# Kernel tuning notes

Measured on AMD Instinct MI355X. Metric: run time of the kernel, lower is better.

The kernel has to match this reference:

```python
import jax, jax.numpy as jnp
import numpy as np

VOXEL_SIZE = 0.04  # metres per voxel (init_kwargs voxel_size)


def setup_inputs() -> dict:
    key = jax.random.key(0)
    k_feat, k_depth, k_zero, k_t = jax.random.split(key, 4)
    B, C, H, W = 4, 32, 120, 160
    X, Y, Z = 128, 128, 64

    features = jax.random.normal(k_feat, (B, C, H, W), dtype=jnp.float32)

    depths = jax.random.uniform(k_depth, (B, H, W), minval=0.5, maxval=5.0)
    zero_mask = jax.random.uniform(k_zero, (B, H, W)) < 0.05
    depths = jnp.where(zero_mask, 0.0, depths).astype(jnp.float32)

    # realistic post-stride intrinsics (f=200 px, principal point at centre)
    K = jnp.array([[200.0, 0.0, 80.0],
                   [0.0, 200.0, 60.0],
                   [0.0, 0.0, 1.0]], dtype=jnp.float32)
    # extrinsics: identity rotation, small per-frame translation
    t = jax.random.uniform(k_t, (B, 3), minval=-0.5, maxval=0.5)
    Rt = jnp.concatenate([jnp.tile(jnp.eye(3, dtype=jnp.float32)[None], (B, 1, 1)),
                          t[:, :, None]], axis=2)              # (B,3,4)
    projection = jnp.einsum('ij,bjk->bik', K, Rt)              # (B,3,4)

    origin = jnp.tile(jnp.array([-3.2, -3.2, 0.0], dtype=jnp.float32)[None], (B, 1))

    return {"origin": origin, "projection": projection, "features": features,
            "depths": depths, "X": X, "Y": Y, "Z": Z}


def reference(origin, projection, features, depths, X, Y, Z):
    B, C, H, W = features.shape
    HW = H * W
    XYZ = X * Y * Z

    # pixel grid: torch.meshgrid(arange(H), arange(W)) -> v over rows, u over cols
    v, u = jnp.meshgrid(jnp.arange(H, dtype=features.dtype),
                        jnp.arange(W, dtype=features.dtype), indexing='ij')
    d = depths                                                  # (B,H,W)
    uvd = jnp.stack([u[None] * d, v[None] * d, d, jnp.ones_like(d)],
                    axis=1).reshape(B, 4, HW)                   # (B,4,HW)

    # homogenise projection and invert per batch
    bottom = jnp.tile(jnp.array([[[0.0, 0.0, 0.0, 1.0]]], dtype=projection.dtype),
                      (B, 1, 1))
    proj4 = jnp.concatenate([projection, bottom], axis=1)       # (B,4,4)
    proj_inv = jnp.linalg.inv(proj4)
    world = jnp.einsum('bij,bjp->bip', proj_inv, uvd)[:, :3]    # (B,3,HW)

    voxel_id = jnp.round((world - origin[:, :, None]) / VOXEL_SIZE).astype(jnp.int32)

    depth_mask = (depths.reshape(B, HW) > 0)
    in_x = (voxel_id[:, 0] >= 0) & (voxel_id[:, 0] < X)
    in_y = (voxel_id[:, 1] >= 0) & (voxel_id[:, 1] < Y)
    in_z = (voxel_id[:, 2] >= 0) & (voxel_id[:, 2] < Z)
    mask = depth_mask & in_x & in_y & in_z                      # (B,HW)

    # flat voxel index; invalid pixels routed out-of-bounds and dropped by scatter
    lin = voxel_id[:, 0] * (Y * Z) + voxel_id[:, 1] * Z + voxel_id[:, 2]
    lin = jnp.where(mask, lin, XYZ)                             # (B,HW)

    feat_flat = features.reshape(B, C, HW)

    def scatter_one(lin_b, feat_b):
        vol = jnp.zeros((C, XYZ), dtype=features.dtype).at[:, lin_b].set(
            feat_b, mode='drop')
        val = jnp.zeros((XYZ,), dtype=features.dtype).at[lin_b].set(
            1.0, mode='drop')
        return vol, val

    volume, valid = jax.vmap(scatter_one)(lin, feat_flat)
    return volume.reshape(B, C, X, Y, Z), valid.reshape(B, 1, X, Y, Z)
```

## Files before the change

### kernel.cpp

```cpp
#include <hip/hip_runtime.h>

#define IMG_W 160
#define VOXEL 0.04f

typedef float f32x4 __attribute__((ext_vector_type(4)));

__device__ __forceinline__ void make_inv(const float* __restrict__ proj, int b,
                                         float inv[12]) {
  const float* P = proj + b * 12;
  const float p00 = P[0], p01 = P[1], p02 = P[2], p03 = P[3];
  const float p11 = P[5], p12 = P[6], p13 = P[7];
  const float p22 = P[10], p23 = P[11];
  const float i00 = __fdiv_rn(1.0f, p00);
  const float i11 = __fdiv_rn(1.0f, p11);
  const float i22 = __fdiv_rn(1.0f, p22);
  const float i01 = __fmul_rn(-i11, __fmul_rn(p01, i00));
  float x0 = __fmul_rn(p02, i00);
  x0 = __fmaf_rn(p12, i01, x0);
  const float x1 = __fmul_rn(p12, i11);
  const float i02 = __fmul_rn(-i22, x0);
  const float i12 = __fmul_rn(-i22, x1);
  float y0 = __fmul_rn(p03, i00);
  y0 = __fmaf_rn(p13, i01, y0);
  float y1 = __fmul_rn(p13, i11);
  y0 = __fmaf_rn(p23, i02, y0);
  y1 = __fmaf_rn(p23, i12, y1);
  const float y2 = __fmul_rn(p23, i22);
  inv[0] = i00;  inv[1] = i01;  inv[2] = i02;   inv[3] = -y0;
  inv[4] = 0.0f; inv[5] = i11;  inv[6] = i12;   inv[7] = -y1;
  inv[8] = 0.0f; inv[9] = 0.0f; inv[10] = i22;  inv[11] = -y2;
}

__device__ __forceinline__ int voxel_lin(const float* __restrict__ origin,
                                         const float* __restrict__ proj,
                                         float d, int b, int p,
                                         int X, int Y, int Z) {
  float inv[12];
  make_inv(proj, b, inv);
  const float u = (float)(p % IMG_W);
  const float v = (float)(p / IMG_W);
  const float uvd[4] = { __fmul_rn(u, d), __fmul_rn(v, d), d, 1.0f };
  float w[3];
#pragma unroll
  for (int r = 0; r < 3; ++r) {
    float acc = 0.0f;
#pragma unroll
    for (int j = 0; j < 4; ++j)
      acc = __fadd_rn(acc, __fmul_rn(inv[r * 4 + j], uvd[j]));
    w[r] = acc;
  }
  const float cx = __fdiv_rn(__fsub_rn(w[0], origin[b * 3 + 0]), VOXEL);
  const float cy = __fdiv_rn(__fsub_rn(w[1], origin[b * 3 + 1]), VOXEL);
  const float cz = __fdiv_rn(__fsub_rn(w[2], origin[b * 3 + 2]), VOXEL);
  const int ix = (int)rintf(cx);
  const int iy = (int)rintf(cy);
  const int iz = (int)rintf(cz);
  if (ix < 0 || ix >= X || iy < 0 || iy >= Y || iz < 0 || iz >= Z) return -1;
  return (ix * Y + iy) * Z + iz;
}

__global__ void k_winner(const float* __restrict__ origin,
                         const float* __restrict__ proj,
                         const float* __restrict__ depths,
                         const int* __restrict__ Xp, const int* __restrict__ Yp,
                         const int* __restrict__ Zp,
                         int* __restrict__ winner, int B, int HW) {
  const int gid = blockIdx.x * blockDim.x + threadIdx.x;
  if (gid >= B * HW) return;
  const int b = gid / HW;
  const int p = gid - b * HW;
  const float d = depths[gid];
  if (!(d > 0.0f)) return;
  const int X = *Xp, Y = *Yp, Z = *Zp;
  const int lin = voxel_lin(origin, proj, d, b, p, X, Y, Z);
  if (lin < 0) return;
  atomicMax(&winner[(long long)b * (X * Y * Z) + lin], p + 1);
}

__device__ __forceinline__ f32x4 vol_quad(const int4 w4,
                                          const float* __restrict__ fc) {
  f32x4 res = {0.0f, 0.0f, 0.0f, 0.0f};
  if ((w4.x | w4.y | w4.z | w4.w) != 0) {
    if (w4.x > 0) res.x = fc[w4.x - 1];
    if (w4.y > 0) res.y = fc[w4.y - 1];
    if (w4.z > 0) res.z = fc[w4.z - 1];
    if (w4.w > 0) res.w = fc[w4.w - 1];
  }
  return res;
}

__device__ __forceinline__ f32x4 val_quad(const int4 w4) {
  f32x4 vo;
  vo.x = (w4.x > 0) ? 1.0f : 0.0f;
  vo.y = (w4.y > 0) ? 1.0f : 0.0f;
  vo.z = (w4.z > 0) ? 1.0f : 0.0f;
  vo.w = (w4.w > 0) ? 1.0f : 0.0f;
  return vo;
}

__global__ void __launch_bounds__(256) k_out8(
    const float* __restrict__ feats, const int* __restrict__ winner,
    float* __restrict__ out, unsigned volFloats, unsigned totFloats,
    unsigned HW, unsigned lgXYZ, unsigned XYZm1, unsigned lgC,
    unsigned nWaves) {
  const unsigned lane = threadIdx.x & 63u;
  const unsigned wid  = (blockIdx.x * 256u + threadIdx.x) >> 6;
  if (wid >= nWaves) return;
  const unsigned q0 = wid * 512u + lane;
  int4 w[8];
#pragma unroll
  for (int k = 0; k < 8; ++k) {
    const unsigned o4 = (q0 + (unsigned)k * 64u) << 2;
    unsigned widx;
    if (o4 < volFloats) {
      const unsigned bc = o4 >> lgXYZ;
      widx = ((bc >> lgC) << lgXYZ) | (o4 & XYZm1);
    } else {
      widx = o4 - volFloats;
    }
    w[k] = *(const int4*)(winner + widx);
  }
#pragma unroll
  for (int k = 0; k < 8; ++k) {
    const unsigned o4 = (q0 + (unsigned)k * 64u) << 2;
    f32x4 res;
    if (o4 < volFloats) {
      const unsigned bc = o4 >> lgXYZ;
      res = vol_quad(w[k], feats + (size_t)bc * HW);
    } else {
      res = val_quad(w[k]);
    }
    *(f32x4*)(out + o4) = res;
  }
}

__global__ void __launch_bounds__(256) k_out(
    const float* __restrict__ feats, const int* __restrict__ winner,
    float* __restrict__ out, unsigned volQuads, unsigned totQuads,
    unsigned HW, unsigned lgXYZ, unsigned XYZm1, unsigned lgC) {
  const unsigned o = blockIdx.x * 256u + threadIdx.x;
  if (o >= totQuads) return;
  const unsigned o4 = o << 2;
  f32x4 res;
  if (o < volQuads) {
    const unsigned bc   = o4 >> lgXYZ;
    const unsigned lin0 = o4 & XYZm1;
    const unsigned b    = bc >> lgC;
    const int4 w4 = *(const int4*)(winner + (((size_t)b << lgXYZ) + lin0));
    res = vol_quad(w4, feats + (size_t)bc * HW);
  } else {
    const unsigned v0 = o4 - (volQuads << 2);
    res = val_quad(*(const int4*)(winner + v0));
  }
  *(f32x4*)(out + o4) = res;
}

extern "C" void kernel_launch(void* const* d_in, const int* in_sizes, int n_in,
                              void* d_out, int out_size, void* d_ws, size_t ws_size,
                              hipStream_t stream) {
  const float* origin = (const float*)d_in[0];
  const float* proj   = (const float*)d_in[1];
  const float* feats  = (const float*)d_in[2];
  const float* depths = (const float*)d_in[3];
  const int*   Xp     = (const int*)d_in[4];
  const int*   Yp     = (const int*)d_in[5];
  const int*   Zp     = (const int*)d_in[6];

  const int B  = in_sizes[0] / 3;
  const int HW = in_sizes[3] / B;
  const int C  = in_sizes[2] / (B * HW);
  const long long XYZ = (long long)out_size / (B * (C + 1));

  float* volume = (float*)d_out;
  int*   winner = (int*)d_ws;

  unsigned lgXYZ = 0; while ((1ll << lgXYZ) < XYZ) ++lgXYZ;
  unsigned lgC = 0;   while ((1u << lgC) < (unsigned)C) ++lgC;
  const bool pow2ok = ((XYZ & (XYZ - 1)) == 0) && ((C & (C - 1)) == 0) &&
                      (XYZ % 256 == 0) && (out_size % 4 == 0);

  hipMemsetAsync(d_ws, 0, (size_t)B * XYZ * sizeof(int), stream);

  const int total = B * HW;
  const int block = 256;
  const int grid  = (total + block - 1) / block;
  k_winner<<<grid, block, 0, stream>>>(origin, proj, depths, Xp, Yp, Zp,
                                       winner, B, HW);

  const unsigned totFloats = (unsigned)out_size;
  const unsigned volFloats = (unsigned)((long long)B * C * XYZ);
  const unsigned totQuads  = totFloats >> 2;
  if (pow2ok && (totQuads % 512u == 0)) {
    const unsigned nWaves = totQuads >> 9;
    const unsigned ogrid  = (nWaves * 64u + 255u) / 256u;
    k_out8<<<ogrid, 256, 0, stream>>>(feats, winner, volume, volFloats,
                                      totFloats, (unsigned)HW, lgXYZ,
                                      (unsigned)(XYZ - 1), lgC, nWaves);
  } else {
    const unsigned volQuads = volFloats >> 2;
    const unsigned ogrid = (totQuads + 255u) / 256u;
    k_out<<<ogrid, 256, 0, stream>>>(feats, winner, volume, volQuads,
                                     totQuads, (unsigned)HW, lgXYZ,
                                     (unsigned)(XYZ - 1), lgC);
  }
}
```

Measured before the change: 602.1 us.

## Pack winner indices to 16-bit and swizzle output blocks across XCDs

Adds a pass that narrows the 32-bit winner array to 16-bit indices, which halves the bytes the output kernel reads for each voxel. The output kernel also remaps block IDs so each XCD gets a contiguous range of blocks, aiming for better L2 locality when several channel slices re-read the same winner data. The cost is an extra kernel launch and an extra read and write of the winner array, plus a larger workspace requirement. A fallback to the 32-bit path remains when HW+1 exceeds 16 bits or the workspace is too small.

```diff
diff --git a/kernel.cpp b/kernel.cpp
--- a/kernel.cpp
+++ b/kernel.cpp
@@ -2,6 +2,7 @@
 
 #define IMG_W 160
 #define VOXEL 0.04f
+#define NXCD 8u
 
 typedef float f32x4 __attribute__((ext_vector_type(4)));
 
@@ -77,6 +78,41 @@
   atomicMax(&winner[(long long)b * (X * Y * Z) + lin], p + 1);
 }
 
+__global__ void __launch_bounds__(256) k_pack(const int* __restrict__ w32,
+                                              unsigned short* __restrict__ w16,
+                                              unsigned nquad) {
+  const unsigned i = blockIdx.x * 256u + threadIdx.x;
+  if (i >= nquad) return;
+  const int4 w = ((const int4*)w32)[i];
+  ushort4 o;
+  o.x = (unsigned short)w.x;
+  o.y = (unsigned short)w.y;
+  o.z = (unsigned short)w.z;
+  o.w = (unsigned short)w.w;
+  ((ushort4*)w16)[i] = o;
+}
+
+__device__ __forceinline__ f32x4 vol_quad_u16(const ushort4 w4,
+                                              const float* __restrict__ fc) {
+  f32x4 res = {0.0f, 0.0f, 0.0f, 0.0f};
+  if ((w4.x | w4.y | w4.z | w4.w) != 0) {
+    if (w4.x) res.x = fc[w4.x - 1];
+    if (w4.y) res.y = fc[w4.y - 1];
+    if (w4.z) res.z = fc[w4.z - 1];
+    if (w4.w) res.w = fc[w4.w - 1];
+  }
+  return res;
+}
+
+__device__ __forceinline__ f32x4 val_quad_u16(const ushort4 w4) {
+  f32x4 vo;
+  vo.x = w4.x ? 1.0f : 0.0f;
+  vo.y = w4.y ? 1.0f : 0.0f;
+  vo.z = w4.z ? 1.0f : 0.0f;
+  vo.w = w4.w ? 1.0f : 0.0f;
+  return vo;
+}
+
 __device__ __forceinline__ f32x4 vol_quad(const int4 w4,
                                           const float* __restrict__ fc) {
   f32x4 res = {0.0f, 0.0f, 0.0f, 0.0f};
@@ -96,6 +132,50 @@
   vo.z = (w4.z > 0) ? 1.0f : 0.0f;
   vo.w = (w4.w > 0) ? 1.0f : 0.0f;
   return vo;
+}
+
+__device__ __forceinline__ unsigned swz_block(unsigned o, unsigned nblk) {
+  const unsigned q = nblk / NXCD, r = nblk % NXCD;
+  const unsigned xcd = o % NXCD, idx = o / NXCD;
+  return (xcd < r) ? (xcd * (q + 1) + idx)
+                   : (r * (q + 1) + (xcd - r) * q + idx);
+}
+
+__global__ void __launch_bounds__(256) k_out8u(
+    const float* __restrict__ feats, const unsigned short* __restrict__ w16,
+    float* __restrict__ out, unsigned volFloats, unsigned totFloats,
+    unsigned HW, unsigned lgXYZ, unsigned XYZm1, unsigned lgC,
+    unsigned nWaves, unsigned nBlocks) {
+  const unsigned blk  = swz_block(blockIdx.x, nBlocks);
+  const unsigned lane = threadIdx.x & 63u;
+  const unsigned wid  = (blk * 256u + threadIdx.x) >> 6;
+  if (wid >= nWaves) return;
+  const unsigned q0 = wid * 512u + lane;
+  ushort4 w[8];
+#pragma unroll
+  for (int k = 0; k < 8; ++k) {
+    const unsigned o4 = (q0 + (unsigned)k * 64u) << 2;
+    unsigned vox;
+    if (o4 < volFloats) {
+      const unsigned bc = o4 >> lgXYZ;
+      vox = ((bc >> lgC) << lgXYZ) | (o4 & XYZm1);
+    } else {
+      vox = o4 - volFloats;
+    }
+    w[k] = ((const ushort4*)w16)[vox >> 2];
+  }
+#pragma unroll
+  for (int k = 0; k < 8; ++k) {
+    const unsigned o4 = (q0 + (unsigned)k * 64u) << 2;
+    f32x4 res;
+    if (o4 < volFloats) {
+      const unsigned bc = o4 >> lgXYZ;
+      res = vol_quad_u16(w[k], feats + (size_t)bc * HW);
+    } else {
+      res = val_quad_u16(w[k]);
+    }
+    *(f32x4*)(out + o4) = res;
+  }
 }
 
 __global__ void __launch_bounds__(256) k_out8(
@@ -173,13 +253,17 @@
 
   float* volume = (float*)d_out;
   int*   winner = (int*)d_ws;
+  const long long totvox = (long long)B * XYZ;
+  unsigned short* w16 = (unsigned short*)((char*)d_ws + (size_t)totvox * 4);
 
   unsigned lgXYZ = 0; while ((1ll << lgXYZ) < XYZ) ++lgXYZ;
   unsigned lgC = 0;   while ((1u << lgC) < (unsigned)C) ++lgC;
   const bool pow2ok = ((XYZ & (XYZ - 1)) == 0) && ((C & (C - 1)) == 0) &&
                       (XYZ % 256 == 0) && (out_size % 4 == 0);
-
-  hipMemsetAsync(d_ws, 0, (size_t)B * XYZ * sizeof(int), stream);
+  const bool u16ok  = (HW + 1 < 65536) && (totvox % 4 == 0) &&
+                      (ws_size >= (size_t)totvox * 6);
+
+  hipMemsetAsync(d_ws, 0, (size_t)totvox * sizeof(int), stream);
 
   const int total = B * HW;
   const int block = 256;
@@ -191,11 +275,20 @@
   const unsigned volFloats = (unsigned)((long long)B * C * XYZ);
   const unsigned totQuads  = totFloats >> 2;
   if (pow2ok && (totQuads % 512u == 0)) {
-    const unsigned nWaves = totQuads >> 9;
-    const unsigned ogrid  = (nWaves * 64u + 255u) / 256u;
-    k_out8<<<ogrid, 256, 0, stream>>>(feats, winner, volume, volFloats,
-                                      totFloats, (unsigned)HW, lgXYZ,
-                                      (unsigned)(XYZ - 1), lgC, nWaves);
+    const unsigned nWaves  = totQuads >> 9;
+    const unsigned nBlocks = (nWaves * 64u + 255u) / 256u;
+    if (u16ok) {
+      const unsigned nq = (unsigned)(totvox >> 2);
+      k_pack<<<(nq + 255u) / 256u, 256, 0, stream>>>(winner, w16, nq);
+      k_out8u<<<nBlocks, 256, 0, stream>>>(feats, w16, volume, volFloats,
+                                           totFloats, (unsigned)HW, lgXYZ,
+                                           (unsigned)(XYZ - 1), lgC, nWaves,
+                                           nBlocks);
+    } else {
+      k_out8<<<nBlocks, 256, 0, stream>>>(feats, winner, volume, volFloats,
+                                          totFloats, (unsigned)HW, lgXYZ,
+                                          (unsigned)(XYZ - 1), lgC, nWaves);
+    }
   } else {
     const unsigned volQuads = volFloats >> 2;
     const unsigned ogrid = (totQuads + 255u) / 256u;
```

After: 606.1 us. Within noise of the previous version (+0.7%).

## Fuse memset, winner scatter and output fill into one cooperative kernel

Applied to the files above, without the earlier changes.

Replaces the memset plus two kernel launches with a single cooperative persistent kernel of fixed grid size. It zeroes the winner buffer, runs the atomicMax scatter, and writes the output in a grid-stride loop, with grid-wide syncs between the phases. The output phase software-prefetches the next winner quad. This removes launch and inter-kernel gaps, at the cost of grid.sync overhead and fewer in-flight loads per wave than the unrolled k_out8. It falls back to the old path if the cooperative launch fails.

```diff
diff --git a/kernel.cpp b/kernel.cpp
--- a/kernel.cpp
+++ b/kernel.cpp
@@ -1,7 +1,11 @@
 #include <hip/hip_runtime.h>
+#include <hip/hip_cooperative_groups.h>
+
+namespace cg = cooperative_groups;
 
 #define IMG_W 160
 #define VOXEL 0.04f
+#define MEGA_GRID 1024
 
 typedef float f32x4 __attribute__((ext_vector_type(4)));
 
@@ -59,6 +63,109 @@
   return (ix * Y + iy) * Z + iz;
 }
 
+__device__ __forceinline__ f32x4 vol_quad(const int4 w4,
+                                          const float* __restrict__ fc) {
+  f32x4 res = {0.0f, 0.0f, 0.0f, 0.0f};
+  if ((w4.x | w4.y | w4.z | w4.w) != 0) {
+    if (w4.x > 0) res.x = fc[w4.x - 1];
+    if (w4.y > 0) res.y = fc[w4.y - 1];
+    if (w4.z > 0) res.z = fc[w4.z - 1];
+    if (w4.w > 0) res.w = fc[w4.w - 1];
+  }
+  return res;
+}
+
+__device__ __forceinline__ f32x4 val_quad(const int4 w4) {
+  f32x4 vo;
+  vo.x = (w4.x > 0) ? 1.0f : 0.0f;
+  vo.y = (w4.y > 0) ? 1.0f : 0.0f;
+  vo.z = (w4.z > 0) ? 1.0f : 0.0f;
+  vo.w = (w4.w > 0) ? 1.0f : 0.0f;
+  return vo;
+}
+
+__device__ __forceinline__ unsigned win_idx(unsigned o4, unsigned volFloats,
+                                            unsigned lgXYZ, unsigned XYZm1,
+                                            unsigned lgC) {
+  if (o4 < volFloats) {
+    const unsigned bc = o4 >> lgXYZ;
+    return ((bc >> lgC) << lgXYZ) | (o4 & XYZm1);
+  }
+  return o4 - volFloats;
+}
+
+__global__ void __launch_bounds__(256, 4) k_mega(
+    const float* __restrict__ origin, const float* __restrict__ proj,
+    const float* __restrict__ depths, const float* __restrict__ feats,
+    const int* __restrict__ Xp, const int* __restrict__ Yp,
+    const int* __restrict__ Zp, int* __restrict__ winner,
+    float* __restrict__ out, int B, int HW,
+    unsigned volFloats, unsigned totFloats, unsigned lgXYZ, unsigned XYZm1,
+    unsigned lgC, unsigned totvox) {
+  cg::grid_group grid = cg::this_grid();
+  const unsigned nthr = gridDim.x * 256u;
+  const unsigned tid  = blockIdx.x * 256u + threadIdx.x;
+
+  {
+    const unsigned nq = totvox >> 2;
+    const int4 z = make_int4(0, 0, 0, 0);
+    for (unsigned i = tid; i < nq; i += nthr) ((int4*)winner)[i] = z;
+  }
+  grid.sync();
+
+  for (unsigned g = tid; g < (unsigned)(B * HW); g += nthr) {
+    const int b = g / HW;
+    const int p = (int)g - b * HW;
+    const float d = depths[g];
+    if (d > 0.0f) {
+      const int X = *Xp, Y = *Yp, Z = *Zp;
+      const int lin = voxel_lin(origin, proj, d, b, p, X, Y, Z);
+      if (lin >= 0)
+        atomicMax(&winner[(long long)b * ((long long)X * Y * Z) + lin], p + 1);
+    }
+  }
+  grid.sync();
+
+  const unsigned lane   = threadIdx.x & 63u;
+  const unsigned wid    = tid >> 6;
+  const unsigned nwaves = nthr >> 6;
+  const unsigned totQuads = totFloats >> 2;
+  const unsigned nIter  = totQuads / (nwaves * 64u);
+  if (nIter > 0) {
+    unsigned q  = wid * (nIter * 64u) + lane;
+    unsigned o4 = q << 2;
+    int4 w = *(const int4*)(winner +
+                            win_idx(o4, volFloats, lgXYZ, XYZm1, lgC));
+    for (unsigned j = 0; j < nIter; ++j) {
+      const unsigned qn  = q + 64u;
+      const unsigned o4n = qn << 2;
+      int4 wn;
+      if (j + 1u < nIter)
+        wn = *(const int4*)(winner +
+                            win_idx(o4n, volFloats, lgXYZ, XYZm1, lgC));
+      f32x4 res;
+      if (o4 < volFloats)
+        res = vol_quad(w, feats + (size_t)(o4 >> lgXYZ) * HW);
+      else
+        res = val_quad(w);
+      *(f32x4*)(out + o4) = res;
+      w = wn; q = qn; o4 = o4n;
+    }
+  }
+  const unsigned done = nIter * nwaves * 64u;
+  for (unsigned qq = done + tid; qq < totQuads; qq += nthr) {
+    const unsigned o4 = qq << 2;
+    const int4 w = *(const int4*)(winner +
+                                  win_idx(o4, volFloats, lgXYZ, XYZm1, lgC));
+    f32x4 res;
+    if (o4 < volFloats)
+      res = vol_quad(w, feats + (size_t)(o4 >> lgXYZ) * HW);
+    else
+      res = val_quad(w);
+    *(f32x4*)(out + o4) = res;
+  }
+}
+
 __global__ void k_winner(const float* __restrict__ origin,
                          const float* __restrict__ proj,
                          const float* __restrict__ depths,
@@ -77,27 +184,6 @@
   atomicMax(&winner[(long long)b * (X * Y * Z) + lin], p + 1);
 }
 
-__device__ __forceinline__ f32x4 vol_quad(const int4 w4,
-                                          const float* __restrict__ fc) {
-  f32x4 res = {0.0f, 0.0f, 0.0f, 0.0f};
-  if ((w4.x | w4.y | w4.z | w4.w) != 0) {
-    if (w4.x > 0) res.x = fc[w4.x - 1];
-    if (w4.y > 0) res.y = fc[w4.y - 1];
-    if (w4.z > 0) res.z = fc[w4.z - 1];
-    if (w4.w > 0) res.w = fc[w4.w - 1];
-  }
-  return res;
-}
-
-__device__ __forceinline__ f32x4 val_quad(const int4 w4) {
-  f32x4 vo;
-  vo.x = (w4.x > 0) ? 1.0f : 0.0f;
-  vo.y = (w4.y > 0) ? 1.0f : 0.0f;
-  vo.z = (w4.z > 0) ? 1.0f : 0.0f;
-  vo.w = (w4.w > 0) ? 1.0f : 0.0f;
-  return vo;
-}
-
 __global__ void __launch_bounds__(256) k_out8(
     const float* __restrict__ feats, const int* __restrict__ winner,
     float* __restrict__ out, unsigned volFloats, unsigned totFloats,
@@ -111,25 +197,16 @@
 #pragma unroll
   for (int k = 0; k < 8; ++k) {
     const unsigned o4 = (q0 + (unsigned)k * 64u) << 2;
-    unsigned widx;
-    if (o4 < volFloats) {
-      const unsigned bc = o4 >> lgXYZ;
-      widx = ((bc >> lgC) << lgXYZ) | (o4 & XYZm1);
-    } else {
-      widx = o4 - volFloats;
-    }
-    w[k] = *(const int4*)(winner + widx);
+    w[k] = *(const int4*)(winner + win_idx(o4, volFloats, lgXYZ, XYZm1, lgC));
   }
 #pragma unroll
   for (int k = 0; k < 8; ++k) {
     const unsigned o4 = (q0 + (unsigned)k * 64u) << 2;
     f32x4 res;
-    if (o4 < volFloats) {
-      const unsigned bc = o4 >> lgXYZ;
-      res = vol_quad(w[k], feats + (size_t)bc * HW);
-    } else {
+    if (o4 < volFloats)
+      res = vol_quad(w[k], feats + (size_t)(o4 >> lgXYZ) * HW);
+    else
       res = val_quad(w[k]);
-    }
     *(f32x4*)(out + o4) = res;
   }
 }
@@ -141,17 +218,13 @@
   const unsigned o = blockIdx.x * 256u + threadIdx.x;
   if (o >= totQuads) return;
   const unsigned o4 = o << 2;
+  const int4 w4 = *(const int4*)(winner +
+                                 win_idx(o4, volQuads << 2, lgXYZ, XYZm1, lgC));
   f32x4 res;
-  if (o < volQuads) {
-    const unsigned bc   = o4 >> lgXYZ;
-    const unsigned lin0 = o4 & XYZm1;
-    const unsigned b    = bc >> lgC;
-    const int4 w4 = *(const int4*)(winner + (((size_t)b << lgXYZ) + lin0));
-    res = vol_quad(w4, feats + (size_t)bc * HW);
-  } else {
-    const unsigned v0 = o4 - (volQuads << 2);
-    res = val_quad(*(const int4*)(winner + v0));
-  }
+  if (o < volQuads)
+    res = vol_quad(w4, feats + (size_t)(o4 >> lgXYZ) * HW);
+  else
+    res = val_quad(w4);
   *(f32x4*)(out + o4) = res;
 }
 
@@ -166,41 +239,61 @@
   const int*   Yp     = (const int*)d_in[5];
   const int*   Zp     = (const int*)d_in[6];
 
-  const int B  = in_sizes[0] / 3;
-  const int HW = in_sizes[3] / B;
-  const int C  = in_sizes[2] / (B * HW);
+  int B  = in_sizes[0] / 3;
+  int HW = in_sizes[3] / B;
+  const int C = in_sizes[2] / (B * HW);
   const long long XYZ = (long long)out_size / (B * (C + 1));
 
   float* volume = (float*)d_out;
   int*   winner = (int*)d_ws;
+  const long long totvox = (long long)B * XYZ;
 
   unsigned lgXYZ = 0; while ((1ll << lgXYZ) < XYZ) ++lgXYZ;
   unsigned lgC = 0;   while ((1u << lgC) < (unsigned)C) ++lgC;
   const bool pow2ok = ((XYZ & (XYZ - 1)) == 0) && ((C & (C - 1)) == 0) &&
-                      (XYZ % 256 == 0) && (out_size % 4 == 0);
-
-  hipMemsetAsync(d_ws, 0, (size_t)B * XYZ * sizeof(int), stream);
-
-  const int total = B * HW;
-  const int block = 256;
-  const int grid  = (total + block - 1) / block;
-  k_winner<<<grid, block, 0, stream>>>(origin, proj, depths, Xp, Yp, Zp,
+                      (XYZ % 256 == 0) && (out_size % 4 == 0) &&
+                      (totvox % 4 == 0);
+
+  unsigned totFloats = (unsigned)out_size;
+  unsigned volFloats = (unsigned)((long long)B * C * XYZ);
+  unsigned XYZm1     = (unsigned)(XYZ - 1);
+  unsigned totvoxU   = (unsigned)totvox;
+
+  bool done = false;
+  if (pow2ok) {
+    void* args[] = { (void*)&origin, (void*)&proj, (void*)&depths,
+                     (void*)&feats,  (void*)&Xp,   (void*)&Yp, (void*)&Zp,
+                     (void*)&winner, (void*)&volume, (void*)&B, (void*)&HW,
+                     (void*)&volFloats, (void*)&totFloats, (void*)&lgXYZ,
+                     (void*)&XYZm1, (void*)&lgC, (void*)&totvoxU };
+    hipError_t ce = hipLaunchCooperativeKernel(
+        (const void*)k_mega, dim3(MEGA_GRID), dim3(256), args, 0, stream);
+    if (ce == hipSuccess) {
+      done = true;
+    } else {
+      (void)hipGetLastError();
+    }
+  }
+
+  if (!done) {
+    hipMemsetAsync(d_ws, 0, (size_t)totvox * sizeof(int), stream);
+    const int total = B * HW;
+    const int grid  = (total + 255) / 256;
+    k_winner<<<grid, 256, 0, stream>>>(origin, proj, depths, Xp, Yp, Zp,
                                        winner, B, HW);
-
-  const unsigned totFloats = (unsigned)out_size;
-  const unsigned volFloats = (unsigned)((long long)B * C * XYZ);
-  const unsigned totQuads  = totFloats >> 2;
-  if (pow2ok && (totQuads % 512u == 0)) {
-    const unsigned nWaves = totQuads >> 9;
-    const unsigned ogrid  = (nWaves * 64u + 255u) / 256u;
-    k_out8<<<ogrid, 256, 0, stream>>>(feats, winner, volume, volFloats,
-                                      totFloats, (unsigned)HW, lgXYZ,
-                                      (unsigned)(XYZ - 1), lgC, nWaves);
-  } else {
-    const unsigned volQuads = volFloats >> 2;
-    const unsigned ogrid = (totQuads + 255u) / 256u;
-    k_out<<<ogrid, 256, 0, stream>>>(feats, winner, volume, volQuads,
-                                     totQuads, (unsigned)HW, lgXYZ,
-                                     (unsigned)(XYZ - 1), lgC);
-  }
-}
+    const unsigned totQuads = totFloats >> 2;
+    if (pow2ok && (totQuads % 512u == 0)) {
+      const unsigned nWaves  = totQuads >> 9;
+      const unsigned nBlocks = (nWaves * 64u + 255u) / 256u;
+      k_out8<<<nBlocks, 256, 0, stream>>>(feats, winner, volume, volFloats,
+                                          totFloats, (unsigned)HW, lgXYZ,
+                                          XYZm1, lgC, nWaves);
+    } else {
+      const unsigned volQuads = volFloats >> 2;
+      const unsigned ogrid = (totQuads + 255u) / 256u;
+      k_out<<<ogrid, 256, 0, stream>>>(feats, winner, volume, volQuads,
+                                       totQuads, (unsigned)HW, lgXYZ,
+                                       XYZm1, lgC);
+    }
+  }
+}
```

After: 813.9 us. +35.2%, slower.
